# Optimization experiments

Hardware: AMD Instinct MI355X
Metric: run time of the kernel (lower is better)

Reference implementation:

```python
import jax, jax.numpy as jnp
import numpy as np

B, S, H = 2, 2048, 1024
NH, HD = 16, 64            # num heads, head dim
R = 8                      # lora rank
LORA_SCALE = 64.0 / 8.0    # lora_alpha / lora_rank
SCALE = jnp.sqrt(jnp.float32(HD))


def setup_inputs() -> dict:
    key = jax.random.key(0)
    ks = jax.random.split(key, 14)
    std = 1.0 / np.sqrt(H)
    p = {
        'hidden_states': jax.random.normal(ks[0], (B, S, H), jnp.float32),
        'attention_mask': jnp.ones((B, S), jnp.float32),
        # base projections, stored [in, out] so y = x @ W
        'Wq': jax.random.normal(ks[1], (H, H), jnp.float32) * std,
        'Wk': jax.random.normal(ks[2], (H, H), jnp.float32) * std,
        'Wv': jax.random.normal(ks[3], (H, H), jnp.float32) * std,
        'Wo': jax.random.normal(ks[4], (H, H), jnp.float32) * std,
        # LoRA down (A: [H,R]) / up (B: [R,H]) for q,k,v,output
        'Aq': jax.random.normal(ks[5], (H, R), jnp.float32) * 0.01,
        'Bq': jax.random.normal(ks[6], (R, H), jnp.float32) * 0.01,
        'Ak': jax.random.normal(ks[7], (H, R), jnp.float32) * 0.01,
        'Bk': jax.random.normal(ks[8], (R, H), jnp.float32) * 0.01,
        'Av': jax.random.normal(ks[9], (H, R), jnp.float32) * 0.01,
        'Bv': jax.random.normal(ks[10], (R, H), jnp.float32) * 0.01,
        'Ao': jax.random.normal(ks[11], (H, R), jnp.float32) * 0.01,
        'Bo': jax.random.normal(ks[12], (R, H), jnp.float32) * 0.01,
    }
    return p


def _heads(x):
    # [B,S,H] -> [B,NH,S,HD]
    return x.reshape(B, S, NH, HD).transpose(0, 2, 1, 3)


def reference(hidden_states, attention_mask, Wq, Wk, Wv, Wo,
              Aq, Bq, Ak, Bk, Av, Bv, Ao, Bo):
    hs = hidden_states
    sg = jax.lax.stop_gradient  # freeze_base=True: base projections are no_grad

    q = sg(hs @ Wq) + (hs @ Aq) @ Bq * LORA_SCALE
    k = sg(hs @ Wk) + (hs @ Ak) @ Bk * LORA_SCALE
    v = sg(hs @ Wv) + (hs @ Av) @ Bv * LORA_SCALE

    qh, kh, vh = _heads(q), _heads(k), _heads(v)  # [B,NH,S,HD]

    scores = jnp.einsum('bhqd,bhkd->bhqk', qh, kh) / SCALE  # [B,NH,S,S]
    mask = (1.0 - attention_mask)[:, None, None, :] * -10000.0
    scores = scores + mask
    probs = jax.nn.softmax(scores, axis=-1)  # dropout is identity in eval

    ctx = jnp.einsum('bhqk,bhkd->bhqd', probs, vh)
    ctx = ctx.transpose(0, 2, 1, 3).reshape(B, S, H)

    out = sg(ctx @ Wo) + (ctx @ Ao) @ Bo * LORA_SCALE
    return out
```

## Files before the change

kernel.cpp:

```cpp
#include <hip/hip_runtime.h>
#include <math.h>

typedef float fx4 __attribute__((ext_vector_type(4)));
typedef float f32x4 __attribute__((ext_vector_type(4)));
typedef float f32x16 __attribute__((ext_vector_type(16)));
typedef short bf16x8 __attribute__((ext_vector_type(8)));
typedef unsigned short us4 __attribute__((ext_vector_type(4)));
typedef unsigned short us8 __attribute__((ext_vector_type(8)));
typedef unsigned int u32x4 __attribute__((ext_vector_type(4)));

#define HDIM 1024
#define SEQ  2048
#define BATCH 2
#define NHEAD 16
#define HD    64
#define MTOT  4096
#define LSCALE 8.0f
#define LOG2E 1.44269504088896340736f

__device__ __forceinline__ unsigned short f2bf(float f) {
    union { float f; unsigned int u; } v; v.f = f;
    unsigned int r = v.u + 0x7FFFu + ((v.u >> 16) & 1u);
    return (unsigned short)(r >> 16);
}
__device__ __forceinline__ float bf2f(unsigned short h) {
    union { unsigned int u; float f; } v; v.u = ((unsigned int)h) << 16;
    return v.f;
}
__device__ __forceinline__ unsigned int cvt_pk_bf16(float a, float b) {
    unsigned int r;
    asm("v_cvt_pk_bf16_f32 %0, %1, %2" : "=v"(r) : "v"(a), "v"(b));
    return r;
}

__global__ __launch_bounds__(256)
void split_x_kernel(const float* __restrict__ X, unsigned short* __restrict__ Xh,
                    unsigned short* __restrict__ Xl, int n4)
{
    int i = blockIdx.x * 256 + threadIdx.x;
    int stride = gridDim.x * 256;
    for (; i < n4; i += stride) {
        fx4 v = *((const fx4*)X + i);
        us4 h, l;
#pragma unroll
        for (int j = 0; j < 4; ++j) {
            h[j] = f2bf(v[j]);
            l[j] = f2bf(v[j] - bf2f(h[j]));
        }
        *((us4*)Xh + i) = h;
        *((us4*)Xl + i) = l;
    }
}

__global__ __launch_bounds__(256)
void tsplit_w_kernel(const float* __restrict__ W0, const float* __restrict__ W1,
                     const float* __restrict__ W2, const float* __restrict__ W3,
                     unsigned short* __restrict__ WTbase)
{
    int z = blockIdx.z;
    const float* W = (z == 0) ? W0 : (z == 1) ? W1 : (z == 2) ? W2 : W3;
    unsigned short* WTh = WTbase + (size_t)z * 2097152;
    unsigned short* WTl = WTh + 1048576;
    int n0 = blockIdx.x * 64, k0 = blockIdx.y * 64;
    __shared__ unsigned int T[64][65];
    int t = threadIdx.x;
#pragma unroll
    for (int i = 0; i < 4; ++i) {
        int idx = t + 256 * i;
        int r = idx >> 4, c4 = (idx & 15) * 4;
        fx4 w = *(const fx4*)&W[(size_t)(k0 + r) * HDIM + n0 + c4];
#pragma unroll
        for (int j = 0; j < 4; ++j) {
            unsigned short hi = f2bf(w[j]);
            unsigned short lo = f2bf(w[j] - bf2f(hi));
            T[r][c4 + j] = (unsigned int)hi | ((unsigned int)lo << 16);
        }
    }
    __syncthreads();
#pragma unroll
    for (int i = 0; i < 4; ++i) {
        int idx = t + 256 * i;
        int n = idx >> 4, kg = (idx & 15) * 4;
        us4 hv, lv;
#pragma unroll
        for (int j = 0; j < 4; ++j) {
            unsigned int p = T[kg + j][n];
            hv[j] = (unsigned short)(p & 0xffffu);
            lv[j] = (unsigned short)(p >> 16);
        }
        *(us4*)&WTh[(size_t)(n0 + n) * HDIM + k0 + kg] = hv;
        *(us4*)&WTl[(size_t)(n0 + n) * HDIM + k0 + kg] = lv;
    }
}

__global__ __launch_bounds__(64)
void lora_down_kernel(const float* __restrict__ X,
                      const float* __restrict__ A0,
                      const float* __restrict__ A1,
                      const float* __restrict__ A2,
                      float* __restrict__ out, int nmat)
{
    int row  = blockIdx.x;
    int lane = threadIdx.x;
    const float* xr = X + (size_t)row * HDIM;
    float xv[16];
#pragma unroll
    for (int i = 0; i < 16; ++i) xv[i] = xr[lane + 64 * i];
    const float* Amats[3] = {A0, A1, A2};
    for (int m = 0; m < nmat; ++m) {
        const float* A = Amats[m];
        float s[8];
#pragma unroll
        for (int c = 0; c < 8; ++c) s[c] = 0.f;
#pragma unroll
        for (int i = 0; i < 16; ++i) {
            const float* ap = A + (size_t)(lane + 64 * i) * 8;
#pragma unroll
            for (int c = 0; c < 8; ++c) s[c] += xv[i] * ap[c];
        }
#pragma unroll
        for (int c = 0; c < 8; ++c) {
#pragma unroll
            for (int off = 1; off < 64; off <<= 1)
                s[c] += __shfl_xor(s[c], off, 64);
        }
        if (lane == 0) {
#pragma unroll
            for (int c = 0; c < 8; ++c)
                out[(size_t)row * 24 + m * 8 + c] = s[c];
        }
    }
}

__global__ __launch_bounds__(64)
void lora_down_bf_kernel(const unsigned short* __restrict__ Xh,
                         const unsigned short* __restrict__ Xl,
                         const float* __restrict__ A,
                         float* __restrict__ out)
{
    int row  = blockIdx.x;
    int lane = threadIdx.x;
    const unsigned short* xh = Xh + (size_t)row * HDIM;
    const unsigned short* xl = Xl + (size_t)row * HDIM;
    float xv[16];
#pragma unroll
    for (int i = 0; i < 16; ++i)
        xv[i] = bf2f(xh[lane + 64 * i]) + bf2f(xl[lane + 64 * i]);
    float s[8];
#pragma unroll
    for (int c = 0; c < 8; ++c) s[c] = 0.f;
#pragma unroll
    for (int i = 0; i < 16; ++i) {
        const float* ap = A + (size_t)(lane + 64 * i) * 8;
#pragma unroll
        for (int c = 0; c < 8; ++c) s[c] += xv[i] * ap[c];
    }
#pragma unroll
    for (int c = 0; c < 8; ++c) {
#pragma unroll
        for (int off = 1; off < 64; off <<= 1)
            s[c] += __shfl_xor(s[c], off, 64);
    }
    if (lane == 0) {
#pragma unroll
        for (int c = 0; c < 8; ++c) out[(size_t)row * 8 + c] = s[c];
    }
}

template<bool OUTF32, int BM>
__global__ __launch_bounds__(256, BM == 128 ? 2 : 3)
void gemm_mfma_kernel(const unsigned short* __restrict__ Xh, const unsigned short* __restrict__ Xl,
                      const unsigned short* __restrict__ WTbase, int wsel0,
                      const float* __restrict__ XA, int xa_stride, int xa_off0,
                      const float* __restrict__ Bu0, const float* __restrict__ Bu1, const float* __restrict__ Bu2,
                      void* __restrict__ O0, void* __restrict__ O1, void* __restrict__ O2,
                      int vtpz, unsigned short* __restrict__ vtout)
{
    constexpr int FN = (BM == 128) ? 4 : 2;
    int pz = blockIdx.z;
    const unsigned short* WTh = WTbase + (size_t)(wsel0 + pz) * 2097152;
    const unsigned short* WTl = WTh + 1048576;
    const float* Bu = (pz == 0) ? Bu0 : (pz == 1) ? Bu1 : Bu2;
    void* Ovp       = (pz == 0) ? O0 : (pz == 1) ? O1 : O2;
    int xa_off = xa_off0 + pz * 8;

    int brow = blockIdx.y * BM, bcol = blockIdx.x * 128;
    int t = threadIdx.x, wid = t >> 6, lane = t & 63, l15 = lane & 15, g = lane >> 4;
    int wm = (BM == 128) ? (wid >> 1) * 64 : 0;
    int wn = (BM == 128) ? (wid & 1) * 64 : wid * 32;

    __shared__ unsigned short Ah[BM][40];
    __shared__ unsigned short Al[BM][40];
    __shared__ unsigned short Bh[128][40];
    __shared__ unsigned short Bl[128][40];

    f32x4 acc[4][FN];
#pragma unroll
    for (int i = 0; i < 4; ++i)
#pragma unroll
        for (int j = 0; j < FN; ++j) acc[i][j] = (f32x4){0.f, 0.f, 0.f, 0.f};

    int sm = t >> 2, skg = t & 3;
    const unsigned short* aH0 = Xh  + (size_t)(brow + sm) * HDIM + 8 * skg;
    const unsigned short* aL0 = Xl  + (size_t)(brow + sm) * HDIM + 8 * skg;
    const unsigned short* bH0 = WTh + (size_t)(bcol + sm) * HDIM + 8 * skg;
    const unsigned short* bL0 = WTl + (size_t)(bcol + sm) * HDIM + 8 * skg;
    const size_t R64 = (size_t)64 * HDIM;

    us8 rAH0, rAH1, rAL0, rAL1, rBH0, rBH1, rBL0, rBL1;
    rAH0 = *(const us8*)(aH0);
    rAL0 = *(const us8*)(aL0);
    if (BM == 128) {
        rAH1 = *(const us8*)(aH0 + R64);
        rAL1 = *(const us8*)(aL0 + R64);
    }
    rBH0 = *(const us8*)(bH0);
    rBH1 = *(const us8*)(bH0 + R64);
    rBL0 = *(const us8*)(bL0);
    rBL1 = *(const us8*)(bL0 + R64);

    for (int k0 = 0; k0 < HDIM; k0 += 32) {
        __syncthreads();
        *(us8*)&Ah[sm][8 * skg] = rAH0;
        *(us8*)&Al[sm][8 * skg] = rAL0;
        if (BM == 128) {
            *(us8*)&Ah[(sm + 64) & (BM - 1)][8 * skg] = rAH1;
            *(us8*)&Al[(sm + 64) & (BM - 1)][8 * skg] = rAL1;
        }
        *(us8*)&Bh[sm][8 * skg]      = rBH0;
        *(us8*)&Bh[sm + 64][8 * skg] = rBH1;
        *(us8*)&Bl[sm][8 * skg]      = rBL0;
        *(us8*)&Bl[sm + 64][8 * skg] = rBL1;
        __syncthreads();
        if (k0 + 32 < HDIM) {
            int ko = k0 + 32;
            rAH0 = *(const us8*)(aH0 + ko);
            rAL0 = *(const us8*)(aL0 + ko);
            if (BM == 128) {
                rAH1 = *(const us8*)(aH0 + R64 + ko);
                rAL1 = *(const us8*)(aL0 + R64 + ko);
            }
            rBH0 = *(const us8*)(bH0 + ko);
            rBH1 = *(const us8*)(bH0 + R64 + ko);
            rBL0 = *(const us8*)(bL0 + ko);
            rBL1 = *(const us8*)(bL0 + R64 + ko);
        }
        bf16x8 fah[4], fal[4], fbh[FN], fbl[FN];
#pragma unroll
        for (int f = 0; f < 4; ++f) {
            fah[f] = *(const bf16x8*)&Ah[wm + 16 * f + l15][8 * g];
            fal[f] = *(const bf16x8*)&Al[wm + 16 * f + l15][8 * g];
        }
#pragma unroll
        for (int f = 0; f < FN; ++f) {
            fbh[f] = *(const bf16x8*)&Bh[wn + 16 * f + l15][8 * g];
            fbl[f] = *(const bf16x8*)&Bl[wn + 16 * f + l15][8 * g];
        }
#pragma unroll
        for (int fm = 0; fm < 4; ++fm)
#pragma unroll
            for (int fn = 0; fn < FN; ++fn) {
                f32x4 a = acc[fm][fn];
                a = __builtin_amdgcn_mfma_f32_16x16x32_bf16(fah[fm], fbh[fn], a, 0, 0, 0);
                a = __builtin_amdgcn_mfma_f32_16x16x32_bf16(fah[fm], fbl[fn], a, 0, 0, 0);
                a = __builtin_amdgcn_mfma_f32_16x16x32_bf16(fal[fm], fbh[fn], a, 0, 0, 0);
                acc[fm][fn] = a;
            }
    }

    float lb[8][FN];
#pragma unroll
    for (int rr = 0; rr < 8; ++rr)
#pragma unroll
        for (int fn = 0; fn < FN; ++fn)
            lb[rr][fn] = Bu[(size_t)rr * HDIM + bcol + wn + 16 * fn + l15] * LSCALE;

#pragma unroll
    for (int fm = 0; fm < 4; ++fm) {
        float la[4][8];
#pragma unroll
        for (int r = 0; r < 4; ++r) {
            int row = brow + wm + 16 * fm + 4 * g + r;
            const float* lap = XA + (size_t)row * xa_stride + xa_off;
            fx4 q0 = *(const fx4*)lap;
            fx4 q1 = *(const fx4*)(lap + 4);
#pragma unroll
            for (int j = 0; j < 4; ++j) { la[r][j] = q0[j]; la[r][4 + j] = q1[j]; }
        }
#pragma unroll
        for (int fn = 0; fn < FN; ++fn) {
            float tmp[4];
#pragma unroll
            for (int r = 0; r < 4; ++r) {
                float sum = acc[fm][fn][r];
#pragma unroll
                for (int rr = 0; rr < 8; ++rr) sum += la[r][rr] * lb[rr][fn];
                tmp[r] = sum;
            }
            int col  = bcol + wn + 16 * fn + l15;
            int rowb = brow + wm + 16 * fm + 4 * g;
            if (pz == vtpz) {
                int hh = col >> 6, d = col & 63;
                int bb = rowb >> 11, ss = rowb & 2047;
                us4 hv;
#pragma unroll
                for (int r = 0; r < 4; ++r) hv[r] = f2bf(tmp[r]);
                *(us4*)&vtout[(size_t)((bb * NHEAD + hh) * HD + d) * SEQ + ss] = hv;
            } else if (OUTF32) {
#pragma unroll
                for (int r = 0; r < 4; ++r)
                    ((float*)Ovp)[(size_t)(rowb + r) * HDIM + col] = tmp[r];
            } else {
#pragma unroll
                for (int r = 0; r < 4; ++r)
                    ((unsigned short*)Ovp)[(size_t)(rowb + r) * HDIM + col] = f2bf(tmp[r]);
            }
        }
    }
}

#define QBLK 128
#define KVB  64
#define NT   (SEQ / KVB)

__global__ __launch_bounds__(256, 2)
void attn_mfma_kernel(const unsigned short* __restrict__ Qg, const unsigned short* __restrict__ Kg,
                      const unsigned short* __restrict__ Vt, const float* __restrict__ mask,
                      unsigned short* __restrict__ Ch, unsigned short* __restrict__ Cl)
{
    int qt = blockIdx.x, hd = blockIdx.y, b = blockIdx.z;
    int t    = threadIdx.x;
    int wid  = t >> 6;
    int lane = t & 63;
    int q31  = lane & 31;
    int g1   = lane >> 5;

    __shared__ __align__(16) unsigned short Ks[2][64][72];
    __shared__ __align__(16) unsigned short Vs[2][64][72];
    __shared__ __align__(16) float Msd[2][64];

    bf16x8 qB[4];
    const unsigned short* qp = Qg + (size_t)(b * SEQ + qt * QBLK + wid * 32 + q31) * HDIM + hd * HD;
#pragma unroll
    for (int kc = 0; kc < 4; ++kc)
        qB[kc] = *(const bf16x8*)(qp + 16 * kc + 8 * g1);

    float m0 = 0.f;
    f32x4 l4 = (f32x4){0.f, 0.f, 0.f, 0.f};
    f32x16 accO[2];
#pragma unroll
    for (int dh = 0; dh < 2; ++dh)
#pragma unroll
        for (int i = 0; i < 16; ++i) accO[dh][i] = 0.f;

    const unsigned short* kp0 = Kg + (size_t)(b * SEQ) * HDIM + hd * HD;
    const unsigned short* vt0 = Vt + (size_t)((b * NHEAD + hd) * HD) * SEQ;

    const float QSCL = 0.125f * LOG2E;
    const float MSCL = -10000.0f * LOG2E;

    int r0 = t >> 3,           c0 = (t & 7) * 8;
    int r1 = (t + 256) >> 3,   c1 = c0;

    *(us8*)&Ks[0][r0][c0] = *(const us8*)(kp0 + (size_t)r0 * HDIM + c0);
    *(us8*)&Ks[0][r1][c1] = *(const us8*)(kp0 + (size_t)r1 * HDIM + c1);
    *(us8*)&Vs[0][r0][c0] = *(const us8*)(vt0 + (size_t)r0 * SEQ + c0);
    *(us8*)&Vs[0][r1][c1] = *(const us8*)(vt0 + (size_t)r1 * SEQ + c1);
    if (t < 64) Msd[0][t] = (1.0f - mask[b * SEQ + t]) * MSCL;
    __syncthreads();

    int cur = 0;
    for (int kt = 0; kt < NT; ++kt) {
        us8 knr0, knr1, vnr0, vnr1;
        float mreg = 1.0f;
        bool more = (kt + 1 < NT);
        if (more) {
            const unsigned short* kp = kp0 + (size_t)(kt + 1) * KVB * HDIM;
            const unsigned short* vp = vt0 + (kt + 1) * KVB;
            knr0 = *(const us8*)(kp + (size_t)r0 * HDIM + c0);
            knr1 = *(const us8*)(kp + (size_t)r1 * HDIM + c1);
            vnr0 = *(const us8*)(vp + (size_t)r0 * SEQ + c0);
            vnr1 = *(const us8*)(vp + (size_t)r1 * SEQ + c1);
            if (t < 64) mreg = mask[b * SEQ + (kt + 1) * KVB + t];
        }

        f32x16 sQ[2];
#pragma unroll
        for (int kvh = 0; kvh < 2; ++kvh) {
            f32x16 a;
#pragma unroll
            for (int i = 0; i < 16; ++i) a[i] = 0.f;
#pragma unroll
            for (int kc = 0; kc < 4; ++kc) {
                bf16x8 kA = *(const bf16x8*)&Ks[cur][32 * kvh + q31][16 * kc + 8 * g1];
                a = __builtin_amdgcn_mfma_f32_32x32x16_bf16(kA, qB[kc], a, 0, 0, 0);
            }
            sQ[kvh] = a;
        }

#pragma unroll
        for (int kvh = 0; kvh < 2; ++kvh)
#pragma unroll
            for (int hh = 0; hh < 4; ++hh) {
                fx4 msk = *(const fx4*)&Msd[cur][32 * kvh + 8 * hh + 4 * g1];
#pragma unroll
                for (int r = 0; r < 4; ++r)
                    sQ[kvh][4 * hh + r] = fmaf(sQ[kvh][4 * hh + r], QSCL, msk[r]);
            }

        if (kt == 0) {
            float mx = sQ[0][0];
#pragma unroll
            for (int kvh = 0; kvh < 2; ++kvh)
#pragma unroll
                for (int i = 0; i < 16; ++i) mx = fmaxf(mx, sQ[kvh][i]);
            mx = fmaxf(mx, __shfl_xor(mx, 32, 64));
            m0 = fmaxf(mx, -64.f);
        }

#pragma unroll
        for (int kvh = 0; kvh < 2; ++kvh)
#pragma unroll
            for (int hh = 0; hh < 4; ++hh)
#pragma unroll
                for (int r = 0; r < 4; ++r) {
                    float p = exp2f(sQ[kvh][4 * hh + r] - m0);
                    sQ[kvh][4 * hh + r] = p;
                    l4[r] += p;
                }

        unsigned int pkx[2][4], pky[2][4];
#pragma unroll
        for (int kvh = 0; kvh < 2; ++kvh)
#pragma unroll
            for (int hh = 0; hh < 4; ++hh) {
                pkx[kvh][hh] = cvt_pk_bf16(sQ[kvh][4 * hh + 0], sQ[kvh][4 * hh + 1]);
                pky[kvh][hh] = cvt_pk_bf16(sQ[kvh][4 * hh + 2], sQ[kvh][4 * hh + 3]);
            }

        bf16x8 pB[4];
#pragma unroll
        for (int kvh = 0; kvh < 2; ++kvh)
#pragma unroll
            for (int kc2 = 0; kc2 < 2; ++kc2) {
                unsigned int x0 = pkx[kvh][2 * kc2], x1 = pkx[kvh][2 * kc2 + 1];
                unsigned int y0 = pky[kvh][2 * kc2], y1 = pky[kvh][2 * kc2 + 1];
                asm("v_permlane32_swap_b32 %0, %1" : "+v"(x0), "+v"(x1));
                asm("v_permlane32_swap_b32 %0, %1" : "+v"(y0), "+v"(y1));
                u32x4 dd;
                dd[0] = x0; dd[1] = y0; dd[2] = x1; dd[3] = y1;
                pB[2 * kvh + kc2] = *(bf16x8*)&dd;
            }

#pragma unroll
        for (int dh = 0; dh < 2; ++dh) {
            f32x16 a = accO[dh];
#pragma unroll
            for (int kcp = 0; kcp < 4; ++kcp) {
                bf16x8 vA = *(const bf16x8*)&Vs[cur][32 * dh + q31][16 * kcp + 8 * g1];
                a = __builtin_amdgcn_mfma_f32_32x32x16_bf16(vA, pB[kcp], a, 0, 0, 0);
            }
            accO[dh] = a;
        }

        if (more) {
            *(us8*)&Ks[cur ^ 1][r0][c0] = knr0;
            *(us8*)&Ks[cur ^ 1][r1][c1] = knr1;
            *(us8*)&Vs[cur ^ 1][r0][c0] = vnr0;
            *(us8*)&Vs[cur ^ 1][r1][c1] = vnr1;
            if (t < 64) Msd[cur ^ 1][t] = (1.0f - mreg) * MSCL;
        }
        __syncthreads();
        cur ^= 1;
    }

    float l = (l4[0] + l4[1]) + (l4[2] + l4[3]);
    l += __shfl_xor(l, 32, 64);
    float inv = 1.0f / l;
    size_t row = (size_t)(b * SEQ + qt * QBLK + wid * 32 + q31);
#pragma unroll
    for (int dh = 0; dh < 2; ++dh)
#pragma unroll
        for (int hh = 0; hh < 4; ++hh) {
            us4 hv, lv;
#pragma unroll
            for (int r = 0; r < 4; ++r) {
                float o = accO[dh][4 * hh + r] * inv;
                unsigned short hi = f2bf(o);
                hv[r] = hi;
                lv[r] = f2bf(o - bf2f(hi));
            }
            size_t idx = row * HDIM + hd * HD + 32 * dh + 8 * hh + 4 * g1;
            *(us4*)&Ch[idx] = hv;
            *(us4*)&Cl[idx] = lv;
        }
}

extern "C" void kernel_launch(void* const* d_in, const int* in_sizes, int n_in,
                              void* d_out, int out_size, void* d_ws, size_t ws_size,
                              hipStream_t stream)
{
    const float* hs   = (const float*)d_in[0];
    const float* mask = (const float*)d_in[1];
    const float* Wq = (const float*)d_in[2];
    const float* Wk = (const float*)d_in[3];
    const float* Wv = (const float*)d_in[4];
    const float* Wo = (const float*)d_in[5];
    const float* Aq = (const float*)d_in[6];
    const float* Bq = (const float*)d_in[7];
    const float* Ak = (const float*)d_in[8];
    const float* Bk = (const float*)d_in[9];
    const float* Av = (const float*)d_in[10];
    const float* Bv = (const float*)d_in[11];
    const float* Ao = (const float*)d_in[12];
    const float* Bo = (const float*)d_in[13];
    float* out = (float*)d_out;

    char* w = (char*)d_ws;
    unsigned short* Xh = (unsigned short*)(w);
    unsigned short* Xl = (unsigned short*)(w + ((size_t)8 << 20));
    unsigned short* WT = (unsigned short*)(w + ((size_t)16 << 20));
    unsigned short* qb = (unsigned short*)(w + ((size_t)32 << 20));
    unsigned short* kb = (unsigned short*)(w + ((size_t)40 << 20));
    unsigned short* vt = (unsigned short*)(w + ((size_t)56 << 20));
    float* hsA  = (float*)(w + ((size_t)64 << 20));
    float* ctxA = (float*)(w + ((size_t)64 << 20) + 400 * 1024);

    split_x_kernel<<<2048, 256, 0, stream>>>(hs, Xh, Xl, MTOT * HDIM / 4);
    tsplit_w_kernel<<<dim3(16, 16, 4), 256, 0, stream>>>(Wq, Wk, Wv, Wo, WT);
    lora_down_kernel<<<MTOT, 64, 0, stream>>>(hs, Aq, Ak, Av, hsA, 3);
    gemm_mfma_kernel<false, 128><<<dim3(8, 32, 3), 256, 0, stream>>>(
        Xh, Xl, WT, 0, hsA, 24, 0, Bq, Bk, Bv, qb, kb, nullptr, 2, vt);
    attn_mfma_kernel<<<dim3(SEQ / QBLK, NHEAD, BATCH), 256, 0, stream>>>(
        qb, kb, vt, mask, Xh , Xl );
    lora_down_bf_kernel<<<MTOT, 64, 0, stream>>>(Xh, Xl, Ao, ctxA);
    gemm_mfma_kernel<true, 64><<<dim3(8, 64, 1), 256, 0, stream>>>(
        Xh, Xl, WT, 3, ctxA, 8, 0, Bo, Bo, Bo, out, out, out, -1, nullptr);
}
```

Before: 228.5 us.

## Split V transpose into separate kernel and interleave QKV projections in grid

```diff
diff --git a/kernel.cpp b/kernel.cpp
--- a/kernel.cpp
+++ b/kernel.cpp
@@ -93,6 +93,34 @@
     }
 }
 
+__global__ __launch_bounds__(256)
+void transpose_v_kernel(const unsigned short* __restrict__ vb,
+                        unsigned short* __restrict__ vt)
+{
+    int s0 = blockIdx.x * 64;
+    int bh = blockIdx.y;
+    int b = bh >> 4, h = bh & 15;
+    __shared__ unsigned short T[64][80];
+    int t = threadIdx.x;
+#pragma unroll
+    for (int i = 0; i < 2; ++i) {
+        int u = t + 256 * i;
+        int r = u >> 3, cg = u & 7;
+        us8 v = *(const us8*)&vb[(size_t)(b * SEQ + s0 + r) * HDIM + h * HD + 8 * cg];
+        *(us8*)&T[r][8 * cg] = v;
+    }
+    __syncthreads();
+#pragma unroll
+    for (int i = 0; i < 2; ++i) {
+        int u = t + 256 * i;
+        int d = u & 63, sg = u >> 6;
+        us8 v;
+#pragma unroll
+        for (int j = 0; j < 8; ++j) v[j] = T[8 * sg + j][d];
+        *(us8*)&vt[(size_t)(bh * HD + d) * SEQ + s0 + 8 * sg] = v;
+    }
+}
+
 __global__ __launch_bounds__(64)
 void lora_down_kernel(const float* __restrict__ X,
                       const float* __restrict__ A0,
@@ -167,24 +195,25 @@
     }
 }
 
-template<bool OUTF32, int BM>
+template<bool OUTF32, int BM, int ZM>
 __global__ __launch_bounds__(256, BM == 128 ? 2 : 3)
 void gemm_mfma_kernel(const unsigned short* __restrict__ Xh, const unsigned short* __restrict__ Xl,
                       const unsigned short* __restrict__ WTbase, int wsel0,
                       const float* __restrict__ XA, int xa_stride, int xa_off0,
                       const float* __restrict__ Bu0, const float* __restrict__ Bu1, const float* __restrict__ Bu2,
-                      void* __restrict__ O0, void* __restrict__ O1, void* __restrict__ O2,
-                      int vtpz, unsigned short* __restrict__ vtout)
+                      void* __restrict__ O0, void* __restrict__ O1, void* __restrict__ O2)
 {
     constexpr int FN = (BM == 128) ? 4 : 2;
-    int pz = blockIdx.z;
+    int pz, byy;
+    if (ZM > 1) { pz = blockIdx.y % ZM; byy = blockIdx.y / ZM; }
+    else        { pz = blockIdx.z;      byy = blockIdx.y; }
     const unsigned short* WTh = WTbase + (size_t)(wsel0 + pz) * 2097152;
     const unsigned short* WTl = WTh + 1048576;
     const float* Bu = (pz == 0) ? Bu0 : (pz == 1) ? Bu1 : Bu2;
     void* Ovp       = (pz == 0) ? O0 : (pz == 1) ? O1 : O2;
     int xa_off = xa_off0 + pz * 8;
 
-    int brow = blockIdx.y * BM, bcol = blockIdx.x * 128;
+    int brow = byy * BM, bcol = blockIdx.x * 128;
     int t = threadIdx.x, wid = t >> 6, lane = t & 63, l15 = lane & 15, g = lane >> 4;
     int wm = (BM == 128) ? (wid >> 1) * 64 : 0;
     int wn = (BM == 128) ? (wid & 1) * 64 : wid * 32;
@@ -288,34 +317,17 @@
             for (int j = 0; j < 4; ++j) { la[r][j] = q0[j]; la[r][4 + j] = q1[j]; }
         }
 #pragma unroll
-        for (int fn = 0; fn < FN; ++fn) {
-            float tmp[4];
+        for (int fn = 0; fn < FN; ++fn)
 #pragma unroll
             for (int r = 0; r < 4; ++r) {
                 float sum = acc[fm][fn][r];
 #pragma unroll
                 for (int rr = 0; rr < 8; ++rr) sum += la[r][rr] * lb[rr][fn];
-                tmp[r] = sum;
-            }
-            int col  = bcol + wn + 16 * fn + l15;
-            int rowb = brow + wm + 16 * fm + 4 * g;
-            if (pz == vtpz) {
-                int hh = col >> 6, d = col & 63;
-                int bb = rowb >> 11, ss = rowb & 2047;
-                us4 hv;
-#pragma unroll
-                for (int r = 0; r < 4; ++r) hv[r] = f2bf(tmp[r]);
-                *(us4*)&vtout[(size_t)((bb * NHEAD + hh) * HD + d) * SEQ + ss] = hv;
-            } else if (OUTF32) {
-#pragma unroll
-                for (int r = 0; r < 4; ++r)
-                    ((float*)Ovp)[(size_t)(rowb + r) * HDIM + col] = tmp[r];
-            } else {
-#pragma unroll
-                for (int r = 0; r < 4; ++r)
-                    ((unsigned short*)Ovp)[(size_t)(rowb + r) * HDIM + col] = f2bf(tmp[r]);
-            }
-        }
+                size_t row = (size_t)(brow + wm + 16 * fm + 4 * g + r);
+                int col = bcol + wn + 16 * fn + l15;
+                if (OUTF32) ((float*)Ovp)[row * HDIM + col] = sum;
+                else ((unsigned short*)Ovp)[row * HDIM + col] = f2bf(sum);
+            }
     }
 }
 
@@ -522,6 +534,7 @@
     unsigned short* WT = (unsigned short*)(w + ((size_t)16 << 20));
     unsigned short* qb = (unsigned short*)(w + ((size_t)32 << 20));
     unsigned short* kb = (unsigned short*)(w + ((size_t)40 << 20));
+    unsigned short* vb = (unsigned short*)(w + ((size_t)48 << 20));
     unsigned short* vt = (unsigned short*)(w + ((size_t)56 << 20));
     float* hsA  = (float*)(w + ((size_t)64 << 20));
     float* ctxA = (float*)(w + ((size_t)64 << 20) + 400 * 1024);
@@ -529,11 +542,12 @@
     split_x_kernel<<<2048, 256, 0, stream>>>(hs, Xh, Xl, MTOT * HDIM / 4);
     tsplit_w_kernel<<<dim3(16, 16, 4), 256, 0, stream>>>(Wq, Wk, Wv, Wo, WT);
     lora_down_kernel<<<MTOT, 64, 0, stream>>>(hs, Aq, Ak, Av, hsA, 3);
-    gemm_mfma_kernel<false, 128><<<dim3(8, 32, 3), 256, 0, stream>>>(
-        Xh, Xl, WT, 0, hsA, 24, 0, Bq, Bk, Bv, qb, kb, nullptr, 2, vt);
+    gemm_mfma_kernel<false, 128, 3><<<dim3(8, 96), 256, 0, stream>>>(
+        Xh, Xl, WT, 0, hsA, 24, 0, Bq, Bk, Bv, qb, kb, vb);
+    transpose_v_kernel<<<dim3(SEQ / 64, BATCH * NHEAD), 256, 0, stream>>>(vb, vt);
     attn_mfma_kernel<<<dim3(SEQ / QBLK, NHEAD, BATCH), 256, 0, stream>>>(
         qb, kb, vt, mask, Xh , Xl );
     lora_down_bf_kernel<<<MTOT, 64, 0, stream>>>(Xh, Xl, Ao, ctxA);
-    gemm_mfma_kernel<true, 64><<<dim3(8, 64, 1), 256, 0, stream>>>(
-        Xh, Xl, WT, 3, ctxA, 8, 0, Bo, Bo, Bo, out, out, out, -1, nullptr);
-}
+    gemm_mfma_kernel<true, 64, 1><<<dim3(8, 64, 1), 256, 0, stream>>>(
+        Xh, Xl, WT, 3, ctxA, 8, 0, Bo, Bo, Bo, out, out, out);
+}
```

New measurement: 224.2 us. About the same (-1.9%).
